# Kernel tuning notes

Hardware: AMD Instinct MI355X
Metric: run time of the kernel (lower is better)

## Reference

```python
import jax, jax.numpy as jnp
import numpy as np

B, T, C, H = 2, 2048, 1024, 16
HD = C // H
EPS = 1e-5


def setup_inputs() -> dict:
    key = jax.random.key(0)
    ks = jax.random.split(key, 16)
    s = 0.02
    return {
        "x": jax.random.normal(ks[0], (B, T, C), jnp.float32),
        "ln1_w": jnp.ones((C,), jnp.float32),
        "ln1_b": jnp.zeros((C,), jnp.float32),
        "ln2_w": jnp.ones((C,), jnp.float32),
        "ln2_b": jnp.zeros((C,), jnp.float32),
        "Wq": jax.random.normal(ks[1], (C, C), jnp.float32) * s,
        "bq": jnp.zeros((C,), jnp.float32),
        "Wk": jax.random.normal(ks[2], (C, C), jnp.float32) * s,
        "bk": jnp.zeros((C,), jnp.float32),
        "Wv": jax.random.normal(ks[3], (C, C), jnp.float32) * s,
        "bv": jnp.zeros((C,), jnp.float32),
        "Wp": jax.random.normal(ks[4], (C, C), jnp.float32) * s,
        "bp": jnp.zeros((C,), jnp.float32),
        "W1": jax.random.normal(ks[5], (4 * C, C), jnp.float32) * s,
        "b1": jnp.zeros((4 * C,), jnp.float32),
        "W2": jax.random.normal(ks[6], (C, 4 * C), jnp.float32) * s,
        "b2": jnp.zeros((C,), jnp.float32),
    }


def _ln(x, w, b):
    mu = jnp.mean(x, axis=-1, keepdims=True)
    var = jnp.mean((x - mu) ** 2, axis=-1, keepdims=True)
    return (x - mu) * jax.lax.rsqrt(var + EPS) * w + b


def _heads(t):  # (B,T,C) -> (B,H,T,HD)
    return t.reshape(B, T, H, HD).transpose(0, 2, 1, 3)


def reference(x, ln1_w, ln1_b, ln2_w, ln2_b, Wq, bq, Wk, bk, Wv, bv, Wp, bp, W1, b1, W2, b2):
    h = _ln(x, ln1_w, ln1_b)
    q = _heads(h @ Wq.T + bq)
    k = _heads(h @ Wk.T + bk)
    v = _heads(h @ Wv.T + bv)
    att = jnp.einsum("bhqd,bhkd->bhqk", q, k) * (1.0 / np.sqrt(HD))
    causal = jnp.tril(jnp.ones((T, T), bool))
    att = jnp.where(causal, att, -jnp.inf)
    att = jax.nn.softmax(att, axis=-1)
    y = jnp.einsum("bhqk,bhkd->bhqd", att, v)
    y = y.transpose(0, 2, 1, 3).reshape(B, T, C)
    x = x + (y @ Wp.T + bp)
    h2 = _ln(x, ln2_w, ln2_b)
    m = jax.nn.gelu(h2 @ W1.T + b1, approximate=False)
    x = x + (m @ W2.T + b2)
    return x
```

## Files before the change

### kernel.cpp

```cpp
#include <hip/hip_runtime.h>

#define TB 2
#define TT 2048
#define TC 1024
#define TH 16
#define THD 64
#define LNEPS 1e-5f

typedef _Float16 f16;
typedef __attribute__((ext_vector_type(8))) _Float16 f16x8;
typedef __attribute__((ext_vector_type(4))) _Float16 f16x4;
typedef __attribute__((ext_vector_type(4))) float f32x4;

__device__ __forceinline__ f32x4 mfma_16x16x32(f16x8 a, f16x8 b, f32x4 c) {
    return __builtin_amdgcn_mfma_f32_16x16x32_f16(a, b, c, 0, 0, 0);
}

__device__ __forceinline__ void load_lds16(const f16* g, f16* l) {
    __builtin_amdgcn_global_load_lds(
        (const __attribute__((address_space(1))) unsigned int*)g,
        (__attribute__((address_space(3))) unsigned int*)l, 16, 0, 0);
}

__global__ __launch_bounds__(256) void ln_kernel(const float* __restrict__ x,
                                                 const float* __restrict__ w,
                                                 const float* __restrict__ bsrc,
                                                 f16* __restrict__ out) {
    int row  = blockIdx.x * 4 + (threadIdx.x >> 6);
    int lane = threadIdx.x & 63;
    const float4* xr = (const float4*)(x + (size_t)row * TC);
    float4 v[4];
    float s = 0.f, ss = 0.f;
#pragma unroll
    for (int i = 0; i < 4; i++) {
        v[i] = xr[i * 64 + lane];
        s  += v[i].x + v[i].y + v[i].z + v[i].w;
        ss += v[i].x * v[i].x + v[i].y * v[i].y + v[i].z * v[i].z + v[i].w * v[i].w;
    }
#pragma unroll
    for (int off = 32; off > 0; off >>= 1) {
        s  += __shfl_xor(s, off);
        ss += __shfl_xor(ss, off);
    }
    float mean = s * (1.f / TC);
    float var  = ss * (1.f / TC) - mean * mean;
    float rstd = rsqrtf(var + LNEPS);
    const float4* wv = (const float4*)w;
    const float4* bv = (const float4*)bsrc;
    f16x4* ov = (f16x4*)(out + (size_t)row * TC);
#pragma unroll
    for (int i = 0; i < 4; i++) {
        int idx = i * 64 + lane;
        float4 wc = wv[idx], bc = bv[idx];
        f16x4 o;
        o[0] = (f16)((v[i].x - mean) * rstd * wc.x + bc.x);
        o[1] = (f16)((v[i].y - mean) * rstd * wc.y + bc.y);
        o[2] = (f16)((v[i].z - mean) * rstd * wc.z + bc.z);
        o[3] = (f16)((v[i].w - mean) * rstd * wc.w + bc.w);
        ov[idx] = o;
    }
}

__global__ void cvt_all_kernel(const float* __restrict__ Wq, const float* __restrict__ Wk,
                               const float* __restrict__ Wv, const float* __restrict__ Wp,
                               const float* __restrict__ W1, const float* __restrict__ W2,
                               f16* __restrict__ dst) {
    int i = blockIdx.x * blockDim.x + threadIdx.x;
    const int Q = 262144;
    const float* src;
    int j;
    int s = i >> 18;
    if (s < 4) {
        src = (s == 0) ? Wq : (s == 1) ? Wk : (s == 2) ? Wv : Wp;
        j = i & (Q - 1);
    } else if (s < 8) {
        src = W1; j = i - 4 * Q;
    } else {
        src = W2; j = i - 8 * Q;
    }
    float4 v = ((const float4*)src)[j];
    f16x4 o;
    o[0] = (f16)v.x; o[1] = (f16)v.y; o[2] = (f16)v.z; o[3] = (f16)v.w;
    ((f16x4*)dst)[i] = o;
}

template <int BM, int BN, int EPI>
__global__ __launch_bounds__(256) void gemm_kernel(const f16* __restrict__ A,
                                                   const f16* __restrict__ W,
                                                   const float* __restrict__ bias,
                                                   const float* __restrict__ bias2,
                                                   const float* __restrict__ bias3,
                                                   const float* __restrict__ res,
                                                   void* __restrict__ outp,
                                                   int M, int N, int K) {
    constexpr int BK = 32;
    __shared__ __align__(16) f16 sA[BM * BK];
    __shared__ __align__(16) f16 sB[BN * BK];
    const int t  = threadIdx.x;
    const int m0 = blockIdx.y * BM;
    const int n0 = blockIdx.x * BN;
    const int wid = t >> 6, lane = t & 63;
    const int wr = wid >> 1, wc = wid & 1;
    constexpr int WM = BM / 2, WN = BN / 2;
    constexpr int MI = WM / 16, NI = WN / 16;
    f32x4 acc[MI][NI];
#pragma unroll
    for (int i = 0; i < MI; i++)
#pragma unroll
        for (int j = 0; j < NI; j++) acc[i][j] = (f32x4){0.f, 0.f, 0.f, 0.f};
    const int quad = lane >> 4, l15 = lane & 15;

    for (int k0 = 0; k0 < K; k0 += BK) {
#pragma unroll
        for (int i = 0; i < BM * BK / 2048; i++) {
            int idx = t + i * 256;
            int r = idx >> 2, cb = (idx & 3) << 3;
            load_lds16(&A[(size_t)(m0 + r) * K + k0 + cb], &sA[idx * 8]);
        }
#pragma unroll
        for (int i = 0; i < BN * BK / 2048; i++) {
            int idx = t + i * 256;
            int r = idx >> 2, cb = (idx & 3) << 3;
            load_lds16(&W[(size_t)(n0 + r) * K + k0 + cb], &sB[idx * 8]);
        }
        __syncthreads();
        f16x8 af[MI], bf[NI];
#pragma unroll
        for (int i = 0; i < MI; i++)
            af[i] = *(const f16x8*)&sA[(wr * WM + i * 16 + l15) * BK + quad * 8];
#pragma unroll
        for (int j = 0; j < NI; j++)
            bf[j] = *(const f16x8*)&sB[(wc * WN + j * 16 + l15) * BK + quad * 8];
#pragma unroll
        for (int i = 0; i < MI; i++)
#pragma unroll
            for (int j = 0; j < NI; j++)
                acc[i][j] = mfma_16x16x32(af[i], bf[j], acc[i][j]);
        __syncthreads();
    }

#pragma unroll
    for (int i = 0; i < MI; i++) {
#pragma unroll
        for (int j = 0; j < NI; j++) {
            int col   = n0 + wc * WN + j * 16 + l15;
            int rbase = m0 + wr * WM + i * 16 + quad * 4;
            float bvv;
            if constexpr (EPI == 3)
                bvv = (col < 1024) ? bias[col]
                    : (col < 2048) ? bias2[col - 1024] : bias3[col - 2048];
            else
                bvv = bias[col];
#pragma unroll
            for (int r = 0; r < 4; r++) {
                size_t idx = (size_t)(rbase + r) * N + col;
                float v = acc[i][j][r] + bvv;
                if constexpr (EPI == 0 || EPI == 3) {
                    ((f16*)outp)[idx] = (f16)v;
                } else if constexpr (EPI == 1) {
                    ((float*)outp)[idx] = v + res[idx];
                } else {
                    ((f16*)outp)[idx] = (f16)(0.5f * v * (1.f + erff(v * 0.70710678118f)));
                }
            }
        }
    }
}

__global__ __launch_bounds__(256) void transpose_kernel(const f16* __restrict__ in,
                                                        f16* __restrict__ out) {
    __shared__ f16 tile[32][33];
    int bt = blockIdx.x;
    int b  = bt / (TT / 32);
    int t0 = (bt % (TT / 32)) * 32;
    int c0 = blockIdx.y * 32;
    int tx = threadIdx.x & 31;
    int ty = threadIdx.x >> 5;
    for (int r = ty; r < 32; r += 8)
        tile[r][tx] = in[(size_t)(b * TT + t0 + r) * 3072 + 2048 + c0 + tx];
    __syncthreads();
    for (int r = ty; r < 32; r += 8)
        out[(size_t)(b * TC + c0 + r) * TT + t0 + tx] = tile[tx][r];
}

__global__ __launch_bounds__(256, 4) void attn_kernel(const f16* __restrict__ qkv,
                                                      const f16* __restrict__ vtg,
                                                      f16* __restrict__ yg) {
    __shared__ __align__(16) f16 sK[2][64 * 64];
    __shared__ __align__(16) f16 sV[2][64 * 64];
    __shared__ __align__(16) f16 pl[4][16 * 64];
    const int t    = threadIdx.x;
    const int wid  = t >> 6, lane = t & 63;
    const int quad = lane >> 4, l15 = lane & 15;
    const int idx = blockIdx.x;
    const int u = idx & 255, r = idx >> 8;
    const int bh = u & 31, rc = u >> 5;
    const int qblk = (r == 0) ? rc : (r == 1) ? 31 - rc : (r == 2) ? 8 + rc : 23 - rc;
    const int b = bh >> 4, h = bh & 15;
    const int q0 = qblk * 64;
    const int q0w = q0 + wid * 16;

    const f16* qptr = qkv + (size_t)(b * TT) * 3072 + h * THD;
    const f16* kptr = qptr + 1024;

    f16x8 qa0, qa1;
    {
        const f16* qb_ = qptr + (size_t)(q0w + l15) * 3072 + quad * 8;
        qa0 = *(const f16x8*)qb_;
        qa1 = *(const f16x8*)(qb_ + 32);
#pragma unroll
        for (int j = 0; j < 8; j++) { qa0[j] *= (f16)0.125f; qa1[j] *= (f16)0.125f; }
    }

    auto stage = [&](int buf, int k0) {
#pragma unroll
        for (int i = 0; i < 2; i++) {
            int p = t + i * 256;
            int row = p >> 3, c0 = p & 7;
            int cc = c0 ^ (row & 7);
            load_lds16(kptr + (size_t)(k0 + row) * 3072 + cc * 8, &sK[buf][p * 8]);
            load_lds16(vtg + (size_t)(bh * THD + row) * TT + k0 + cc * 8, &sV[buf][p * 8]);
        }
    };

    f32x4 o[4];
#pragma unroll
    for (int j = 0; j < 4; j++) o[j] = (f32x4){0.f, 0.f, 0.f, 0.f};
    float mcol = -__builtin_inff(), lsum = 0.f;
    f16* plw = pl[wid];
    const int sw = (l15 & 7) << 1;
    const int nt = qblk + 1;

    stage(0, 0);
    for (int it = 0; it < nt; it++) {
        const int cur = it & 1;
        __syncthreads();
        if (it + 1 < nt) stage(cur ^ 1, (it + 1) * 64);
        const int k0 = it * 64;
        if (k0 <= q0w + 15) {
            const f16* sk = sK[cur];
            f32x4 s[4];
#pragma unroll
            for (int g = 0; g < 4; g++) {
                int key = g * 16 + l15;
                f16x8 klo = *(const f16x8*)&sk[(key * 8 + (quad ^ (l15 & 7))) * 8];
                f16x8 khi = *(const f16x8*)&sk[(key * 8 + ((quad + 4) ^ (l15 & 7))) * 8];
                f32x4 a = (f32x4){0.f, 0.f, 0.f, 0.f};
                a = mfma_16x16x32(klo, qa0, a);
                a = mfma_16x16x32(khi, qa1, a);
                s[g] = a;
            }
            const bool full = (k0 + 63 <= q0w);
            float lm = -__builtin_inff();
#pragma unroll
            for (int g = 0; g < 4; g++) {
#pragma unroll
                for (int rr = 0; rr < 4; rr++) {
                    if (!full) {
                        int key = k0 + g * 16 + quad * 4 + rr;
                        if (key > q0w + l15) s[g][rr] = -__builtin_inff();
                    }
                    lm = fmaxf(lm, s[g][rr]);
                }
            }
            lm = fmaxf(lm, __shfl_xor(lm, 16));
            lm = fmaxf(lm, __shfl_xor(lm, 32));
            float mnew  = fmaxf(mcol, lm);
            float alpha = __expf(mcol - mnew);
            mcol = mnew;
            float sum = 0.f;
#pragma unroll
            for (int g = 0; g < 4; g++) {
                f16x4 pw;
#pragma unroll
                for (int rr = 0; rr < 4; rr++) {
                    float p = __expf(s[g][rr] - mnew);
                    sum += p;
                    pw[rr] = (f16)p;
                }
                *(f16x4*)&plw[(l15 * 16 + ((g * 4 + quad) ^ sw)) * 4] = pw;
            }
            sum += __shfl_xor(sum, 16);
            sum += __shfl_xor(sum, 32);
            lsum = lsum * alpha + sum;
#pragma unroll
            for (int j = 0; j < 4; j++) {
                o[j][0] *= alpha; o[j][1] *= alpha; o[j][2] *= alpha; o[j][3] *= alpha;
            }
            __asm__ volatile("s_waitcnt lgkmcnt(0)" ::: "memory");
            const f16* sv = sV[cur];
#pragma unroll
            for (int hh = 0; hh < 2; hh++) {
                f16x8 pb = *(const f16x8*)&plw[(l15 * 16 + ((hh * 8 + quad * 2) ^ sw)) * 4];
#pragma unroll
                for (int j = 0; j < 4; j++) {
                    int d = j * 16 + l15;
                    f16x8 vf = *(const f16x8*)&sv[(d * 8 + ((4 * hh + quad) ^ (l15 & 7))) * 8];
                    o[j] = mfma_16x16x32(vf, pb, o[j]);
                }
            }
        }
    }
    float inv = 1.f / lsum;
    size_t rowbase = (size_t)(b * TT + q0w + l15) * TC + h * THD;
#pragma unroll
    for (int j = 0; j < 4; j++) {
        f16x4 ov;
#pragma unroll
        for (int rr = 0; rr < 4; rr++) ov[rr] = (f16)(o[j][rr] * inv);
        *(f16x4*)&yg[rowbase + j * 16 + quad * 4] = ov;
    }
}

extern "C" void kernel_launch(void* const* d_in, const int* in_sizes, int n_in,
                              void* d_out, int out_size, void* d_ws, size_t ws_size,
                              hipStream_t stream) {
    const float* x    = (const float*)d_in[0];
    const float* ln1w = (const float*)d_in[1];
    const float* ln1b = (const float*)d_in[2];
    const float* ln2w = (const float*)d_in[3];
    const float* ln2b = (const float*)d_in[4];
    const float* Wq   = (const float*)d_in[5];
    const float* bq   = (const float*)d_in[6];
    const float* Wk   = (const float*)d_in[7];
    const float* bk   = (const float*)d_in[8];
    const float* Wv   = (const float*)d_in[9];
    const float* bv   = (const float*)d_in[10];
    const float* Wp   = (const float*)d_in[11];
    const float* bp   = (const float*)d_in[12];
    const float* W1   = (const float*)d_in[13];
    const float* b1   = (const float*)d_in[14];
    const float* W2   = (const float*)d_in[15];
    const float* b2   = (const float*)d_in[16];

    char* ws = (char*)d_ws;
    const size_t MB = 1024 * 1024;
    f16* hb   = (f16*)(ws + 0);
    f16* qkv  = (f16*)(ws + 8 * MB);
    f16* vT   = (f16*)(ws + 32 * MB);
    f16* mb   = (f16*)(ws + 16 * MB);
    f16* Wb   = (f16*)(ws + 48 * MB);
    f16* Wqb  = Wb;
    f16* Wpb  = Wb + (size_t)3 * 1024 * 1024;
    f16* W1b  = Wb + (size_t)4 * 1024 * 1024;
    f16* W2b  = Wb + (size_t)8 * 1024 * 1024;
    f16* yb   = hb;
    f16* h2b  = qkv;
    float* x1 = (float*)d_out;

    cvt_all_kernel<<<12288, 256, 0, stream>>>(Wq, Wk, Wv, Wp, W1, W2, Wb);
    ln_kernel<<<1024, 256, 0, stream>>>(x, ln1w, ln1b, hb);

    gemm_kernel<128, 128, 3><<<dim3(3072 / 128, (TB * TT) / 128), 256, 0, stream>>>(
        hb, Wqb, bq, bk, bv, nullptr, qkv, TB * TT, 3072, TC);
    transpose_kernel<<<dim3(TB * TT / 32, TC / 32), 256, 0, stream>>>(qkv, vT);
    attn_kernel<<<1024, 256, 0, stream>>>(qkv, vT, yb);
    gemm_kernel<128, 64, 1><<<dim3(TC / 64, (TB * TT) / 128), 256, 0, stream>>>(
        yb, Wpb, bp, nullptr, nullptr, x, x1, TB * TT, TC, TC);
    ln_kernel<<<1024, 256, 0, stream>>>(x1, ln2w, ln2b, h2b);
    gemm_kernel<128, 128, 2><<<dim3(4 * TC / 128, (TB * TT) / 128), 256, 0, stream>>>(
        h2b, W1b, b1, nullptr, nullptr, nullptr, mb, TB * TT, 4 * TC, TC);
    gemm_kernel<128, 64, 1><<<dim3(TC / 64, (TB * TT) / 128), 256, 0, stream>>>(
        mb, W2b, b2, nullptr, nullptr, x1, x1, TB * TT, TC, 4 * TC);
}
```

Baseline: 396.3 us.

## Swizzle GEMM LDS layout and split-K the W2 projection with reduction kernel

The GEMM stores its LDS tiles with an XOR-like rotation of the 16-byte column chunks per row pair, so the fragment reads avoid LDS bank conflicts. The final MLP down-projection switches from a 128x64 tile to 128x128 tiles and splits K=4096 into two halves across blockIdx.z. Each half writes an fp16 partial, and a new reduction kernel sums the partials with the bias and the residual. The split raises the tile size without dropping the block count. It costs an extra kernel launch and a partial-buffer round trip, and storing the partials in fp16 loses some precision.

```diff
diff --git a/kernel.cpp b/kernel.cpp
--- a/kernel.cpp
+++ b/kernel.cpp
@@ -103,6 +103,14 @@
     const int wr = wid >> 1, wc = wid & 1;
     constexpr int WM = BM / 2, WN = BN / 2;
     constexpr int MI = WM / 16, NI = WN / 16;
+    int kbeg = 0, kstop = K;
+    f16* pout = (f16*)outp;
+    if constexpr (EPI == 4) {
+        int Ks = K >> 1;
+        kbeg = blockIdx.z * Ks;
+        kstop = kbeg + Ks;
+        pout += (size_t)blockIdx.z * M * N;
+    }
     f32x4 acc[MI][NI];
 #pragma unroll
     for (int i = 0; i < MI; i++)
@@ -110,27 +118,33 @@
         for (int j = 0; j < NI; j++) acc[i][j] = (f32x4){0.f, 0.f, 0.f, 0.f};
     const int quad = lane >> 4, l15 = lane & 15;
 
-    for (int k0 = 0; k0 < K; k0 += BK) {
-#pragma unroll
-        for (int i = 0; i < BM * BK / 2048; i++) {
-            int idx = t + i * 256;
-            int r = idx >> 2, cb = (idx & 3) << 3;
-            load_lds16(&A[(size_t)(m0 + r) * K + k0 + cb], &sA[idx * 8]);
-        }
-#pragma unroll
-        for (int i = 0; i < BN * BK / 2048; i++) {
-            int idx = t + i * 256;
-            int r = idx >> 2, cb = (idx & 3) << 3;
-            load_lds16(&W[(size_t)(n0 + r) * K + k0 + cb], &sB[idx * 8]);
+    for (int k0 = kbeg; k0 < kstop; k0 += BK) {
+#pragma unroll
+        for (int i = 0; i < BM * 4 / 256; i++) {
+            int p = t + i * 256;
+            int row = p >> 2, pc = p & 3;
+            int c = (pc - (row >> 1)) & 3;
+            load_lds16(&A[(size_t)(m0 + row) * K + k0 + c * 8], &sA[p * 8]);
+        }
+#pragma unroll
+        for (int i = 0; i < BN * 4 / 256; i++) {
+            int p = t + i * 256;
+            int row = p >> 2, pc = p & 3;
+            int c = (pc - (row >> 1)) & 3;
+            load_lds16(&W[(size_t)(n0 + row) * K + k0 + c * 8], &sB[p * 8]);
         }
         __syncthreads();
         f16x8 af[MI], bf[NI];
 #pragma unroll
-        for (int i = 0; i < MI; i++)
-            af[i] = *(const f16x8*)&sA[(wr * WM + i * 16 + l15) * BK + quad * 8];
-#pragma unroll
-        for (int j = 0; j < NI; j++)
-            bf[j] = *(const f16x8*)&sB[(wc * WN + j * 16 + l15) * BK + quad * 8];
+        for (int i = 0; i < MI; i++) {
+            int r = wr * WM + i * 16 + l15;
+            af[i] = *(const f16x8*)&sA[(r * 4 + ((quad + (r >> 1)) & 3)) * 8];
+        }
+#pragma unroll
+        for (int j = 0; j < NI; j++) {
+            int r = wc * WN + j * 16 + l15;
+            bf[j] = *(const f16x8*)&sB[(r * 4 + ((quad + (r >> 1)) & 3)) * 8];
+        }
 #pragma unroll
         for (int i = 0; i < MI; i++)
 #pragma unroll
@@ -145,11 +159,11 @@
         for (int j = 0; j < NI; j++) {
             int col   = n0 + wc * WN + j * 16 + l15;
             int rbase = m0 + wr * WM + i * 16 + quad * 4;
-            float bvv;
+            float bvv = 0.f;
             if constexpr (EPI == 3)
                 bvv = (col < 1024) ? bias[col]
                     : (col < 2048) ? bias2[col - 1024] : bias3[col - 2048];
-            else
+            else if constexpr (EPI != 4)
                 bvv = bias[col];
 #pragma unroll
             for (int r = 0; r < 4; r++) {
@@ -159,12 +173,30 @@
                     ((f16*)outp)[idx] = (f16)v;
                 } else if constexpr (EPI == 1) {
                     ((float*)outp)[idx] = v + res[idx];
+                } else if constexpr (EPI == 2) {
+                    ((f16*)outp)[idx] = (f16)(0.5f * v * (1.f + erff(v * 0.70710678118f)));
                 } else {
-                    ((f16*)outp)[idx] = (f16)(0.5f * v * (1.f + erff(v * 0.70710678118f)));
+                    pout[idx] = (f16)v;
                 }
             }
         }
     }
+}
+
+__global__ __launch_bounds__(256) void reduce2_kernel(const f16* __restrict__ part,
+                                                      const float* __restrict__ b2,
+                                                      float* __restrict__ x1) {
+    int i = blockIdx.x * 256 + threadIdx.x;
+    const f16x4* p0 = (const f16x4*)part;
+    const f16x4* p1 = p0 + (1 << 20);
+    f16x4 a = p0[i], b = p1[i];
+    float4 r = ((float4*)x1)[i];
+    float4 bb = ((const float4*)b2)[i & 255];
+    r.x += (float)a[0] + (float)b[0] + bb.x;
+    r.y += (float)a[1] + (float)b[1] + bb.y;
+    r.z += (float)a[2] + (float)b[2] + bb.z;
+    r.w += (float)a[3] + (float)b[3] + bb.w;
+    ((float4*)x1)[i] = r;
 }
 
 __global__ __launch_bounds__(256) void transpose_kernel(const f16* __restrict__ in,
@@ -346,6 +378,7 @@
     f16* W2b  = Wb + (size_t)8 * 1024 * 1024;
     f16* yb   = hb;
     f16* h2b  = qkv;
+    f16* part = hb;
     float* x1 = (float*)d_out;
 
     cvt_all_kernel<<<12288, 256, 0, stream>>>(Wq, Wk, Wv, Wp, W1, W2, Wb);
@@ -360,6 +393,7 @@
     ln_kernel<<<1024, 256, 0, stream>>>(x1, ln2w, ln2b, h2b);
     gemm_kernel<128, 128, 2><<<dim3(4 * TC / 128, (TB * TT) / 128), 256, 0, stream>>>(
         h2b, W1b, b1, nullptr, nullptr, nullptr, mb, TB * TT, 4 * TC, TC);
-    gemm_kernel<128, 64, 1><<<dim3(TC / 64, (TB * TT) / 128), 256, 0, stream>>>(
-        mb, W2b, b2, nullptr, nullptr, x1, x1, TB * TT, TC, 4 * TC);
-}
+    gemm_kernel<128, 128, 4><<<dim3(TC / 128, (TB * TT) / 128, 2), 256, 0, stream>>>(
+        mb, W2b, nullptr, nullptr, nullptr, nullptr, part, TB * TT, TC, 4 * TC);
+    reduce2_kernel<<<4096, 256, 0, stream>>>(part, b2, x1);
+}
```

Measured after the change: 392.2 us. Within noise of the previous version (-1.0%).
